# Kernel tuning notes

Measured on AMD Instinct MI355X. Metric: run time of the kernel, lower is better.

Reference implementation:

```python
import jax, jax.numpy as jnp
import numpy as np

B, S, D, H = 4, 2048, 1024, 16
DH = D // H
DFF = 4 * D
EPS = 1e-7


def _layernorm(x, scale, shift):
    # Note original quirk: (normalized + shift) * scale, biased variance, eps=1e-7
    m = jnp.mean(x, axis=-1, keepdims=True)
    v = jnp.mean((x - m) ** 2, axis=-1, keepdims=True)
    return ((x - m) / jnp.sqrt(v + EPS) + shift) * scale


def _gelu(x):
    c = jnp.sqrt(jnp.asarray(2.0 / jnp.pi, dtype=x.dtype))
    return 0.5 * x * (1.0 + jnp.tanh(c * (x + 0.044715 * x ** 3)))


def setup_inputs() -> dict:
    key = jax.random.key(0)
    ks = jax.random.split(key, 8)
    s = 0.02
    return {
        "x": jax.random.normal(ks[0], (B, S, D), jnp.float32),
        "Wq": jax.random.normal(ks[1], (D, D), jnp.float32) * s,
        "Wk": jax.random.normal(ks[2], (D, D), jnp.float32) * s,
        "Wv": jax.random.normal(ks[3], (D, D), jnp.float32) * s,
        "Wo": jax.random.normal(ks[4], (D, D), jnp.float32) * s,
        "bo": jnp.zeros((D,), jnp.float32),
        "W1": jax.random.normal(ks[5], (DFF, D), jnp.float32) * s,
        "b1": jnp.zeros((DFF,), jnp.float32),
        "W2": jax.random.normal(ks[6], (D, DFF), jnp.float32) * s,
        "b2": jnp.zeros((D,), jnp.float32),
        "ln1_scale": jnp.ones((D,), jnp.float32),
        "ln1_shift": jnp.zeros((D,), jnp.float32),
        "ln2_scale": jnp.ones((D,), jnp.float32),
        "ln2_shift": jnp.zeros((D,), jnp.float32),
    }


def reference(x, Wq, Wk, Wv, Wo, bo, W1, b1, W2, b2,
              ln1_scale, ln1_shift, ln2_scale, ln2_shift):
    b, s, d = x.shape
    h = _layernorm(x, ln1_scale, ln1_shift)
    # torch Linear: y = h @ W.T
    q = (h @ Wq.T).reshape(b, s, H, DH).transpose(0, 2, 1, 3)  # bhsd
    k = (h @ Wk.T).reshape(b, s, H, DH).transpose(0, 2, 1, 3)
    v = (h @ Wv.T).reshape(b, s, H, DH).transpose(0, 2, 1, 3)
    scores = jnp.einsum('bhqd,bhkd->bhqk', q, k) / jnp.sqrt(jnp.asarray(DH, x.dtype))
    causal = jnp.tril(jnp.ones((s, s), dtype=bool))
    scores = jnp.where(causal, scores, -jnp.inf)
    attn = jax.nn.softmax(scores, axis=-1)
    ctx = jnp.einsum('bhqk,bhkd->bhqd', attn, v)
    ctx = ctx.transpose(0, 2, 1, 3).reshape(b, s, d)
    attn_out = ctx @ Wo.T + bo
    x1 = x + attn_out  # residual (dropout is identity at eval / p effectively unused)
    h2 = _layernorm(x1, ln2_scale, ln2_shift)
    ff = _gelu(h2 @ W1.T + b1) @ W2.T + b2
    return x1 + ff
```

## Files before the change

kernel.cpp:

```cpp
#include <hip/hip_runtime.h>
#include <hip/hip_bf16.h>
#include <math.h>

typedef __bf16 bf16;
typedef __bf16 bf16x2_t __attribute__((ext_vector_type(2)));
typedef __bf16 bf16x4_t __attribute__((ext_vector_type(4)));
typedef __bf16 bf16x8_t __attribute__((ext_vector_type(8)));
typedef float  floatx4  __attribute__((ext_vector_type(4)));

#define DEVI static __device__ __forceinline__

constexpr int Bb = 4, Ss = 2048, Dd = 1024, Hh = 16, DHh = 64, DFFc = 4096;
constexpr int NTOK = Bb * Ss;
constexpr int NQKV = 3072;

DEVI void gld_lds16(const void* g, void* l) {
  __builtin_amdgcn_global_load_lds(
      (const __attribute__((address_space(1))) void*)g,
      (__attribute__((address_space(3))) void*)l, 16, 0, 0);
}

DEVI float gelu_f(float x) {
  const float c = 0.7978845608028654f;
  float t = tanhf(c * (x + 0.044715f * x * x * x));
  return 0.5f * x * (1.0f + t);
}

DEVI int xcd_lin(int lin, int nwg) {
  return (lin & 7) * (nwg >> 3) + (lin >> 3);
}

struct CastArgs {
  const float* src[6];
  bf16* dst[6];
  int n[6];
};
__global__ __launch_bounds__(256) void cast_w_kernel(CastArgs a) {
  const int which = blockIdx.y;
  const int idx = (blockIdx.x * 256 + threadIdx.x) * 4;
  if (idx >= a.n[which]) return;
  float4 v = *(const float4*)(a.src[which] + idx);
  bf16x4_t o = {(bf16)v.x, (bf16)v.y, (bf16)v.z, (bf16)v.w};
  *(bf16x4_t*)(a.dst[which] + idx) = o;
}

template <typename TIN>
__global__ __launch_bounds__(256) void ln_kernel(const TIN* __restrict__ x,
                                                 const float* __restrict__ sc,
                                                 const float* __restrict__ sh,
                                                 bf16* __restrict__ out) {
  __shared__ float rs[4], rs2[4];
  const int row = blockIdx.x, t = threadIdx.x;
  const TIN* xr = x + (size_t)row * Dd;
  float v[4];
  if constexpr (sizeof(TIN) == 2) {
    bf16x4_t tmp = *(const bf16x4_t*)((const bf16*)xr + t * 4);
#pragma unroll
    for (int i = 0; i < 4; i++) v[i] = (float)tmp[i];
  } else {
    float4 tmp = *(const float4*)((const float*)xr + t * 4);
    v[0] = tmp.x; v[1] = tmp.y; v[2] = tmp.z; v[3] = tmp.w;
  }
  float s = v[0] + v[1] + v[2] + v[3];
  float s2 = v[0] * v[0] + v[1] * v[1] + v[2] * v[2] + v[3] * v[3];
#pragma unroll
  for (int off = 1; off < 64; off <<= 1) {
    s += __shfl_xor(s, off);
    s2 += __shfl_xor(s2, off);
  }
  if ((t & 63) == 0) { rs[t >> 6] = s; rs2[t >> 6] = s2; }
  __syncthreads();
  float S1 = rs[0] + rs[1] + rs[2] + rs[3];
  float S2 = rs2[0] + rs2[1] + rs2[2] + rs2[3];
  float mean = S1 * (1.0f / Dd);
  float var = S2 * (1.0f / Dd) - mean * mean;
  float rinv = rsqrtf(var + 1e-7f);
#pragma unroll
  for (int i = 0; i < 4; i++) {
    int c = t * 4 + i;
    out[(size_t)row * Dd + c] = (bf16)(((v[i] - mean) * rinv + sh[c]) * sc[c]);
  }
}

template <int BN, int MODE>
__global__ __launch_bounds__(512, 2) void gemmk(const bf16* __restrict__ A,
                                                const bf16* __restrict__ Bw,
                                                const float* __restrict__ bias,
                                                const void* __restrict__ res,
                                                void* __restrict__ outp,
                                                int M, int N, int K) {
  constexpr int BUNITS = BN / 64;
  constexpr int AELEM = 16384;
  constexpr int BELEM = BUNITS * 4096;
  constexpr int WN = (BN == 256) ? 4 : 2;
  constexpr int WM = 8 / WN;
  constexpr int WR_H = 256 / WM;
  constexpr int M_rep = WR_H / 16;
  constexpr int NPH = M_rep / 2;
  __shared__ bf16 lds[2 * (AELEM + BELEM)];
  bf16* Ab = lds;
  bf16* Bl = lds + 2 * AELEM;

  const int tid = threadIdx.x;
  const int w = tid >> 6, lane = tid & 63;
  const int quad = lane >> 4, l16 = lane & 15;
  const int l7x8 = (lane & 7) << 3;
  const int wr = w / WN, wc = w % WN;

  const int gx = (int)gridDim.x;
  const int nwg = gx * (int)gridDim.y;
  const int lin = xcd_lin((int)blockIdx.y * gx + (int)blockIdx.x, nwg);
  const int m0 = (lin / gx) * 256;
  const int n0 = (lin % gx) * BN;

  const int s0 = w * 1024 + lane * 16;
  const int sr = s0 >> 7;
  const int sc = ((s0 ^ ((sr & 7) << 4)) & 127) >> 1;
  const int toff = w * 512 + lane * 8;

  const bf16* Agu[4];
  const bf16* Bgu[BUNITS];
#pragma unroll
  for (int u = 0; u < 4; ++u) Agu[u] = A + (size_t)(m0 + u * 64 + sr) * K + sc;
#pragma unroll
  for (int u = 0; u < BUNITS; ++u)
    Bgu[u] = Bw + (size_t)(n0 + u * 64 + sr) * K + sc;

  auto issA = [&](int t, int lo) {
    const int q = t & 1, ko = t * 64;
#pragma unroll
    for (int u = 0; u < 2; ++u)
      gld_lds16(Agu[lo + u] + ko, Ab + q * AELEM + (lo + u) * 4096 + toff);
  };
  auto issB = [&](int t, int lo, int cnt) {
    const int q = t & 1, ko = t * 64;
#pragma unroll 2
    for (int u = 0; u < cnt; ++u)
      gld_lds16(Bgu[lo + u] + ko, Bl + q * BELEM + (lo + u) * 4096 + toff);
  };

  auto rdA = [&](int q, int mi, int kk) {
    const int r = wr * WR_H + mi * 16 + l16;
    return *(const bf16x8_t*)(Ab + q * AELEM + (r >> 6) * 4096 + (r & 63) * 64 +
                              ((quad * 8 + kk * 32) ^ l7x8));
  };
  auto rdB = [&](int q, int j, int kk) {
    const int r = wc * 64 + j * 16 + l16;
    return *(const bf16x8_t*)(Bl + q * BELEM + (r >> 6) * 4096 + (r & 63) * 64 +
                              ((quad * 8 + kk * 32) ^ l7x8));
  };

  floatx4 acc[M_rep][4] = {};
  const int NT = K >> 6;

  issA(0, 0); issA(0, 2); issB(0, 0, BUNITS);
  issA(1, 0);
  if (BN == 256) {
    issB(1, 0, 2);
    asm volatile("s_waitcnt vmcnt(4)" ::: "memory");
  } else {
    asm volatile("s_waitcnt vmcnt(2)" ::: "memory");
  }
  __builtin_amdgcn_sched_barrier(0);
  __builtin_amdgcn_s_barrier();
  __builtin_amdgcn_sched_barrier(0);

  for (int t = 0; t < NT; ++t) {
    const int q = t & 1;
    bf16x8_t bfv[4][2];
#pragma unroll
    for (int p = 0; p < NPH; ++p) {
      bf16x8_t af[2][2];
#pragma unroll
      for (int im = 0; im < 2; ++im)
#pragma unroll
        for (int kk = 0; kk < 2; ++kk)
          af[im][kk] = rdA(q, p * 2 + im, kk);
      if (p == 0) {
#pragma unroll
        for (int j = 0; j < 4; ++j)
#pragma unroll
          for (int kk = 0; kk < 2; ++kk)
            bfv[j][kk] = rdB(q, j, kk);
        if (t + 1 < NT) {
          issA(t + 1, 2);
          if (BN == 256) issB(t + 1, 2, 2);
          else issB(t + 1, 0, 2);
        }
      }
      __builtin_amdgcn_s_barrier();
      __builtin_amdgcn_sched_barrier(0);
      __builtin_amdgcn_s_setprio(1);
#pragma unroll
      for (int im = 0; im < 2; ++im)
#pragma unroll
        for (int j = 0; j < 4; ++j)
#pragma unroll
          for (int kk = 0; kk < 2; ++kk)
            acc[p * 2 + im][j] = __builtin_amdgcn_mfma_f32_16x16x32_bf16(
                af[im][kk], bfv[j][kk], acc[p * 2 + im][j], 0, 0, 0);
      __builtin_amdgcn_s_setprio(0);
      if (p == NPH - 1) {
        if (t + 2 < NT) {
          issA(t + 2, 0);
          if (BN == 256) issB(t + 2, 0, 2);
          if (BN == 256) asm volatile("s_waitcnt vmcnt(4)" ::: "memory");
          else           asm volatile("s_waitcnt vmcnt(2)" ::: "memory");
        } else {
          asm volatile("s_waitcnt vmcnt(0)" ::: "memory");
        }
        __builtin_amdgcn_sched_barrier(0);
      }
      __builtin_amdgcn_s_barrier();
      __builtin_amdgcn_sched_barrier(0);
    }
  }

#pragma unroll
  for (int i = 0; i < M_rep; ++i) {
    const int rbase = m0 + wr * WR_H + i * 16 + quad * 4;
#pragma unroll
    for (int j2 = 0; j2 < 4; ++j2) {
      const int col = n0 + wc * 64 + j2 * 16 + l16;
      float bv = 0.f;
      if constexpr (MODE == 1 || MODE == 2 || MODE == 3) bv = bias[col];
#pragma unroll
      for (int r = 0; r < 4; ++r) {
        const int row = rbase + r;
        float vacc = acc[i][j2][r] + bv;
        if constexpr (MODE == 0) {
          ((bf16*)outp)[(size_t)row * N + col] = (bf16)vacc;
        } else if constexpr (MODE == 1) {
          float xres = ((const float*)res)[(size_t)row * N + col];
          ((bf16*)outp)[(size_t)row * N + col] = (bf16)(xres + vacc);
        } else if constexpr (MODE == 2) {
          ((bf16*)outp)[(size_t)row * N + col] = (bf16)gelu_f(vacc);
        } else {
          float xres = (float)((const bf16*)res)[(size_t)row * N + col];
          ((float*)outp)[(size_t)row * N + col] = xres + vacc;
        }
      }
    }
  }
}

__global__ __launch_bounds__(256) void attn_kernel(const bf16* __restrict__ QKV,
                                                   bf16* __restrict__ ctx) {
  __shared__ bf16 Ks[64 * 72];
  __shared__ bf16 Vt[64 * 72];
  __shared__ bf16 Ps[4][16 * 72];

  const int tid = threadIdx.x;
  const int wave = tid >> 6, lane = tid & 63;
  const int quad = lane >> 4, l16 = lane & 15;
  const int lin = xcd_lin((int)blockIdx.y * 16 + (int)blockIdx.x, 16 * Bb * Hh);
  const int qb = lin & 15;
  const int bh = lin >> 4;
  const int bsel = bh >> 4, hsel = bh & 15;
  const size_t base = ((size_t)bsel * Ss) * NQKV + (size_t)hsel * 64;
  const bf16* Qp = QKV + base;
  const bf16* Kp = QKV + base + 1024;
  const bf16* Vp = QKV + base + 2048;

  const int kr0 = tid >> 3, kc0 = (tid & 7) * 8;
  const int vp2 = tid & 31, vs = tid >> 5;

  for (int t = 0; t < 2; t++) {
    const int qt = (t == 0) ? qb : 31 - qb;
    const int q0 = qt * 64;

    const int qrow = q0 + wave * 16 + l16;
    bf16x8_t qf0 = *(const bf16x8_t*)(Qp + (size_t)qrow * NQKV + quad * 8);
    bf16x8_t qf1 = *(const bf16x8_t*)(Qp + (size_t)qrow * NQKV + 32 + quad * 8);
#pragma unroll
    for (int i = 0; i < 8; i++) {
      qf0[i] = (bf16)((float)qf0[i] * 0.125f);
      qf1[i] = (bf16)((float)qf1[i] * 0.125f);
    }

    floatx4 o[4] = {};
    float l_i[4] = {0.f, 0.f, 0.f, 0.f};

    {
      bf16x8_t k0 = *(const bf16x8_t*)(Kp + (size_t)kr0 * NQKV + kc0);
      bf16x8_t k1 = *(const bf16x8_t*)(Kp + (size_t)(kr0 + 32) * NQKV + kc0);
      const bf16* v0p = Vp + (size_t)(2 * vp2) * NQKV + vs * 8;
      bf16x8_t va = *(const bf16x8_t*)(v0p);
      bf16x8_t vb = *(const bf16x8_t*)(v0p + NQKV);
      *(bf16x8_t*)(Ks + kr0 * 72 + kc0) = k0;
      *(bf16x8_t*)(Ks + (kr0 + 32) * 72 + kc0) = k1;
#pragma unroll
      for (int i = 0; i < 8; i++) {
        bf16x2_t p2 = {va[i], vb[i]};
        *(bf16x2_t*)(Vt + (vs * 8 + i) * 72 + 2 * vp2) = p2;
      }
      __syncthreads();
    }

    const int ntiles = qt + 1;
    for (int it = 0; it < ntiles; ++it) {
      const int kc = it * 64;
      const bool more = (it + 1) < ntiles;

      bf16x8_t nk0, nk1, nva, nvb;
      if (more) {
        const int kn = kc + 64;
        nk0 = *(const bf16x8_t*)(Kp + (size_t)(kn + kr0) * NQKV + kc0);
        nk1 = *(const bf16x8_t*)(Kp + (size_t)(kn + kr0 + 32) * NQKV + kc0);
        const bf16* v0p = Vp + (size_t)(kn + 2 * vp2) * NQKV + vs * 8;
        nva = *(const bf16x8_t*)(v0p);
        nvb = *(const bf16x8_t*)(v0p + NQKV);
      }

      floatx4 sg[4];
      __builtin_amdgcn_s_setprio(1);
#pragma unroll
      for (int g = 0; g < 4; g++) {
        floatx4 s = {0.f, 0.f, 0.f, 0.f};
        bf16x8_t ka = *(const bf16x8_t*)(Ks + (g * 16 + l16) * 72 + quad * 8);
        bf16x8_t kb = *(const bf16x8_t*)(Ks + (g * 16 + l16) * 72 + 32 + quad * 8);
        s = __builtin_amdgcn_mfma_f32_16x16x32_bf16(qf0, ka, s, 0, 0, 0);
        s = __builtin_amdgcn_mfma_f32_16x16x32_bf16(qf1, kb, s, 0, 0, 0);
        sg[g] = s;
      }
      __builtin_amdgcn_s_setprio(0);

      bf16* pw = &Ps[wave][0];
      const bool diag = (kc == q0);
      if (diag) {
#pragma unroll
        for (int r = 0; r < 4; r++) {
          const int rq = q0 + wave * 16 + quad * 4 + r;
          float p[4];
          float rsum = 0.f;
#pragma unroll
          for (int g = 0; g < 4; g++) {
            float v = (kc + g * 16 + l16 > rq) ? -1e30f : sg[g][r];
            p[g] = __expf(v);
            rsum += p[g];
          }
          rsum += __shfl_xor(rsum, 1);
          rsum += __shfl_xor(rsum, 2);
          rsum += __shfl_xor(rsum, 4);
          rsum += __shfl_xor(rsum, 8);
          l_i[r] += rsum;
#pragma unroll
          for (int g = 0; g < 4; g++)
            pw[(quad * 4 + r) * 72 + g * 16 + l16] = (bf16)p[g];
        }
      } else {
#pragma unroll
        for (int r = 0; r < 4; r++) {
          float p[4];
          float rsum = 0.f;
#pragma unroll
          for (int g = 0; g < 4; g++) {
            p[g] = __expf(sg[g][r]);
            rsum += p[g];
          }
          rsum += __shfl_xor(rsum, 1);
          rsum += __shfl_xor(rsum, 2);
          rsum += __shfl_xor(rsum, 4);
          rsum += __shfl_xor(rsum, 8);
          l_i[r] += rsum;
#pragma unroll
          for (int g = 0; g < 4; g++)
            pw[(quad * 4 + r) * 72 + g * 16 + l16] = (bf16)p[g];
        }
      }

      bf16x8_t pf0 = *(const bf16x8_t*)(pw + l16 * 72 + quad * 8);
      bf16x8_t pf1 = *(const bf16x8_t*)(pw + l16 * 72 + 32 + quad * 8);
      __builtin_amdgcn_s_setprio(1);
#pragma unroll
      for (int nt = 0; nt < 4; nt++) {
        bf16x8_t vf0 = *(const bf16x8_t*)(Vt + (nt * 16 + l16) * 72 + quad * 8);
        bf16x8_t vf1 = *(const bf16x8_t*)(Vt + (nt * 16 + l16) * 72 + 32 + quad * 8);
        o[nt] = __builtin_amdgcn_mfma_f32_16x16x32_bf16(pf0, vf0, o[nt], 0, 0, 0);
        o[nt] = __builtin_amdgcn_mfma_f32_16x16x32_bf16(pf1, vf1, o[nt], 0, 0, 0);
      }
      __builtin_amdgcn_s_setprio(0);

      __syncthreads();
      if (more) {
        *(bf16x8_t*)(Ks + kr0 * 72 + kc0) = nk0;
        *(bf16x8_t*)(Ks + (kr0 + 32) * 72 + kc0) = nk1;
#pragma unroll
        for (int i = 0; i < 8; i++) {
          bf16x2_t p2 = {nva[i], nvb[i]};
          *(bf16x2_t*)(Vt + (vs * 8 + i) * 72 + 2 * vp2) = p2;
        }
        __syncthreads();
      }
    }

#pragma unroll
    for (int nt = 0; nt < 4; nt++)
#pragma unroll
      for (int r = 0; r < 4; r++) {
        const int rq = q0 + wave * 16 + quad * 4 + r;
        size_t a = ((size_t)bsel * Ss + rq) * Dd + (size_t)hsel * DHh + nt * 16 + l16;
        ctx[a] = (bf16)(o[nt][r] / l_i[r]);
      }
  }
}

extern "C" void kernel_launch(void* const* d_in, const int* in_sizes, int n_in,
                              void* d_out, int out_size, void* d_ws, size_t ws_size,
                              hipStream_t stream) {
  (void)in_sizes; (void)n_in; (void)out_size; (void)ws_size;
  const float* x = (const float*)d_in[0];
  const float* Wq = (const float*)d_in[1];
  const float* Wk = (const float*)d_in[2];
  const float* Wv = (const float*)d_in[3];
  const float* Wo = (const float*)d_in[4];
  const float* bo = (const float*)d_in[5];
  const float* W1 = (const float*)d_in[6];
  const float* b1 = (const float*)d_in[7];
  const float* W2 = (const float*)d_in[8];
  const float* b2 = (const float*)d_in[9];
  const float* ln1s = (const float*)d_in[10];
  const float* ln1b = (const float*)d_in[11];
  const float* ln2s = (const float*)d_in[12];
  const float* ln2b = (const float*)d_in[13];

  char* wsb = (char*)d_ws;
  const size_t MB = 1024 * 1024;
  bf16* Wqb = (bf16*)(wsb);
  bf16* Wkb = (bf16*)(wsb + 2 * MB);
  bf16* Wvb = (bf16*)(wsb + 4 * MB);
  bf16* Wob = (bf16*)(wsb + 6 * MB);
  bf16* W1b = (bf16*)(wsb + 8 * MB);
  bf16* W2b = (bf16*)(wsb + 16 * MB);
  bf16* h   = (bf16*)(wsb + 24 * MB);
  bf16* qkv = (bf16*)(wsb + 40 * MB);
  bf16* ctx = (bf16*)(wsb + 88 * MB);
  bf16* x1  = (bf16*)(wsb + 104 * MB);
  bf16* h2  = ctx;
  bf16* ff1 = h;

  dim3 blk(256, 1, 1);
  dim3 blk8(512, 1, 1);

  CastArgs ca;
  ca.src[0] = Wq; ca.src[1] = Wk; ca.src[2] = Wv; ca.src[3] = Wo;
  ca.src[4] = W1; ca.src[5] = W2;
  ca.dst[0] = Wqb; ca.dst[1] = Wkb; ca.dst[2] = Wvb; ca.dst[3] = Wob;
  ca.dst[4] = W1b; ca.dst[5] = W2b;
  ca.n[0] = ca.n[1] = ca.n[2] = ca.n[3] = Dd * Dd;
  ca.n[4] = ca.n[5] = Dd * DFFc;
  cast_w_kernel<<<dim3((Dd * DFFc) / (256 * 4), 6, 1), blk, 0, stream>>>(ca);

  ln_kernel<float><<<dim3(NTOK, 1, 1), blk, 0, stream>>>(x, ln1s, ln1b, h);
  gemmk<256, 0><<<dim3(12, NTOK / 256, 1), blk8, 0, stream>>>(h, Wqb, nullptr, nullptr,
                                                              qkv, NTOK, NQKV, Dd);
  attn_kernel<<<dim3(16, Bb * Hh, 1), blk, 0, stream>>>(qkv, ctx);
  gemmk<128, 1><<<dim3(8, NTOK / 256, 1), blk8, 0, stream>>>(ctx, Wob, bo, x, x1,
                                                             NTOK, Dd, Dd);
  ln_kernel<bf16><<<dim3(NTOK, 1, 1), blk, 0, stream>>>(x1, ln2s, ln2b, h2);
  gemmk<256, 2><<<dim3(16, NTOK / 256, 1), blk8, 0, stream>>>(h2, W1b, b1, nullptr, ff1,
                                                              NTOK, DFFc, Dd);
  gemmk<128, 3><<<dim3(8, NTOK / 256, 1), blk8, 0, stream>>>(ff1, W2b, b2, x1,
                                                             (float*)d_out, NTOK, Dd, DFFc);
}
```

Baseline: 506.9 us.

## Process two adjacent query tiles per attention block to reuse K/V tiles

Each attention block now handles two consecutive 64-row query tiles at once, sharing every staged K/V tile in LDS between both, and balances work by pairing tile group g with 15-g. This halves K/V global loads and LDS staging per query row and halves the grid to 512 blocks. In exchange it raises register pressure (two sets of Q fragments, accumulators and scores), doubles the P scratch in LDS, and lowers the number of blocks available to hide latency.

```diff
diff --git a/kernel.cpp b/kernel.cpp
--- a/kernel.cpp
+++ b/kernel.cpp
@@ -248,14 +248,14 @@
                                                    bf16* __restrict__ ctx) {
   __shared__ bf16 Ks[64 * 72];
   __shared__ bf16 Vt[64 * 72];
-  __shared__ bf16 Ps[4][16 * 72];
+  __shared__ bf16 Ps[4][2][16 * 72];
 
   const int tid = threadIdx.x;
   const int wave = tid >> 6, lane = tid & 63;
   const int quad = lane >> 4, l16 = lane & 15;
-  const int lin = xcd_lin((int)blockIdx.y * 16 + (int)blockIdx.x, 16 * Bb * Hh);
-  const int qb = lin & 15;
-  const int bh = lin >> 4;
+  const int lin = xcd_lin((int)blockIdx.y * 8 + (int)blockIdx.x, 8 * Bb * Hh);
+  const int gsel = lin & 7;
+  const int bh = lin >> 3;
   const int bsel = bh >> 4, hsel = bh & 15;
   const size_t base = ((size_t)bsel * Ss) * NQKV + (size_t)hsel * 64;
   const bf16* Qp = QKV + base;
@@ -265,21 +265,27 @@
   const int kr0 = tid >> 3, kc0 = (tid & 7) * 8;
   const int vp2 = tid & 31, vs = tid >> 5;
 
-  for (int t = 0; t < 2; t++) {
-    const int qt = (t == 0) ? qb : 31 - qb;
-    const int q0 = qt * 64;
-
-    const int qrow = q0 + wave * 16 + l16;
-    bf16x8_t qf0 = *(const bf16x8_t*)(Qp + (size_t)qrow * NQKV + quad * 8);
-    bf16x8_t qf1 = *(const bf16x8_t*)(Qp + (size_t)qrow * NQKV + 32 + quad * 8);
+  for (int pass = 0; pass < 2; ++pass) {
+    const int g2 = (pass == 0) ? gsel : 15 - gsel;
+    const int tA = 2 * g2, tB = tA + 1;
+    const int q0A = tA * 64, q0B = q0A + 64;
+
+    const int qrA = q0A + wave * 16 + l16;
+    const int qrB = q0B + wave * 16 + l16;
+    bf16x8_t qA0 = *(const bf16x8_t*)(Qp + (size_t)qrA * NQKV + quad * 8);
+    bf16x8_t qA1 = *(const bf16x8_t*)(Qp + (size_t)qrA * NQKV + 32 + quad * 8);
+    bf16x8_t qB0 = *(const bf16x8_t*)(Qp + (size_t)qrB * NQKV + quad * 8);
+    bf16x8_t qB1 = *(const bf16x8_t*)(Qp + (size_t)qrB * NQKV + 32 + quad * 8);
 #pragma unroll
     for (int i = 0; i < 8; i++) {
-      qf0[i] = (bf16)((float)qf0[i] * 0.125f);
-      qf1[i] = (bf16)((float)qf1[i] * 0.125f);
+      qA0[i] = (bf16)((float)qA0[i] * 0.125f);
+      qA1[i] = (bf16)((float)qA1[i] * 0.125f);
+      qB0[i] = (bf16)((float)qB0[i] * 0.125f);
+      qB1[i] = (bf16)((float)qB1[i] * 0.125f);
     }
 
-    floatx4 o[4] = {};
-    float l_i[4] = {0.f, 0.f, 0.f, 0.f};
+    floatx4 oA[4] = {}, oB[4] = {};
+    float lA[4] = {0.f, 0.f, 0.f, 0.f}, lB[4] = {0.f, 0.f, 0.f, 0.f};
 
     {
       bf16x8_t k0 = *(const bf16x8_t*)(Kp + (size_t)kr0 * NQKV + kc0);
@@ -297,40 +303,12 @@
       __syncthreads();
     }
 
-    const int ntiles = qt + 1;
-    for (int it = 0; it < ntiles; ++it) {
-      const int kc = it * 64;
-      const bool more = (it + 1) < ntiles;
-
-      bf16x8_t nk0, nk1, nva, nvb;
-      if (more) {
-        const int kn = kc + 64;
-        nk0 = *(const bf16x8_t*)(Kp + (size_t)(kn + kr0) * NQKV + kc0);
-        nk1 = *(const bf16x8_t*)(Kp + (size_t)(kn + kr0 + 32) * NQKV + kc0);
-        const bf16* v0p = Vp + (size_t)(kn + 2 * vp2) * NQKV + vs * 8;
-        nva = *(const bf16x8_t*)(v0p);
-        nvb = *(const bf16x8_t*)(v0p + NQKV);
-      }
-
-      floatx4 sg[4];
-      __builtin_amdgcn_s_setprio(1);
-#pragma unroll
-      for (int g = 0; g < 4; g++) {
-        floatx4 s = {0.f, 0.f, 0.f, 0.f};
-        bf16x8_t ka = *(const bf16x8_t*)(Ks + (g * 16 + l16) * 72 + quad * 8);
-        bf16x8_t kb = *(const bf16x8_t*)(Ks + (g * 16 + l16) * 72 + 32 + quad * 8);
-        s = __builtin_amdgcn_mfma_f32_16x16x32_bf16(qf0, ka, s, 0, 0, 0);
-        s = __builtin_amdgcn_mfma_f32_16x16x32_bf16(qf1, kb, s, 0, 0, 0);
-        sg[g] = s;
-      }
-      __builtin_amdgcn_s_setprio(0);
-
-      bf16* pw = &Ps[wave][0];
-      const bool diag = (kc == q0);
+    auto do_sm = [&](floatx4* sg, float* l_i, bf16* pw, int q0c, bool diag,
+                     int kc) {
       if (diag) {
 #pragma unroll
         for (int r = 0; r < 4; r++) {
-          const int rq = q0 + wave * 16 + quad * 4 + r;
+          const int rq = q0c + wave * 16 + quad * 4 + r;
           float p[4];
           float rsum = 0.f;
 #pragma unroll
@@ -368,16 +346,61 @@
             pw[(quad * 4 + r) * 72 + g * 16 + l16] = (bf16)p[g];
         }
       }
-
-      bf16x8_t pf0 = *(const bf16x8_t*)(pw + l16 * 72 + quad * 8);
-      bf16x8_t pf1 = *(const bf16x8_t*)(pw + l16 * 72 + 32 + quad * 8);
+    };
+
+    const int ntiles = tB + 1;
+    for (int it = 0; it < ntiles; ++it) {
+      const int kc = it * 64;
+      const bool more = (it + 1) < ntiles;
+      const bool aAct = (it <= tA);
+
+      bf16x8_t nk0, nk1, nva, nvb;
+      if (more) {
+        const int kn = kc + 64;
+        nk0 = *(const bf16x8_t*)(Kp + (size_t)(kn + kr0) * NQKV + kc0);
+        nk1 = *(const bf16x8_t*)(Kp + (size_t)(kn + kr0 + 32) * NQKV + kc0);
+        const bf16* v0p = Vp + (size_t)(kn + 2 * vp2) * NQKV + vs * 8;
+        nva = *(const bf16x8_t*)(v0p);
+        nvb = *(const bf16x8_t*)(v0p + NQKV);
+      }
+
+      floatx4 sA[4], sB[4];
+      __builtin_amdgcn_s_setprio(1);
+#pragma unroll
+      for (int g = 0; g < 4; g++) {
+        bf16x8_t ka = *(const bf16x8_t*)(Ks + (g * 16 + l16) * 72 + quad * 8);
+        bf16x8_t kb = *(const bf16x8_t*)(Ks + (g * 16 + l16) * 72 + 32 + quad * 8);
+        floatx4 z = {0.f, 0.f, 0.f, 0.f};
+        if (aAct) {
+          floatx4 s = __builtin_amdgcn_mfma_f32_16x16x32_bf16(qA0, ka, z, 0, 0, 0);
+          sA[g] = __builtin_amdgcn_mfma_f32_16x16x32_bf16(qA1, kb, s, 0, 0, 0);
+        }
+        floatx4 s2 = __builtin_amdgcn_mfma_f32_16x16x32_bf16(qB0, ka, z, 0, 0, 0);
+        sB[g] = __builtin_amdgcn_mfma_f32_16x16x32_bf16(qB1, kb, s2, 0, 0, 0);
+      }
+      __builtin_amdgcn_s_setprio(0);
+
+      if (aAct) do_sm(sA, lA, &Ps[wave][0][0], q0A, it == tA, kc);
+      do_sm(sB, lB, &Ps[wave][1][0], q0B, it == tB, kc);
+
+      bf16x8_t pA0, pA1;
+      if (aAct) {
+        pA0 = *(const bf16x8_t*)(&Ps[wave][0][0] + l16 * 72 + quad * 8);
+        pA1 = *(const bf16x8_t*)(&Ps[wave][0][0] + l16 * 72 + 32 + quad * 8);
+      }
+      bf16x8_t pB0 = *(const bf16x8_t*)(&Ps[wave][1][0] + l16 * 72 + quad * 8);
+      bf16x8_t pB1 = *(const bf16x8_t*)(&Ps[wave][1][0] + l16 * 72 + 32 + quad * 8);
       __builtin_amdgcn_s_setprio(1);
 #pragma unroll
       for (int nt = 0; nt < 4; nt++) {
         bf16x8_t vf0 = *(const bf16x8_t*)(Vt + (nt * 16 + l16) * 72 + quad * 8);
         bf16x8_t vf1 = *(const bf16x8_t*)(Vt + (nt * 16 + l16) * 72 + 32 + quad * 8);
-        o[nt] = __builtin_amdgcn_mfma_f32_16x16x32_bf16(pf0, vf0, o[nt], 0, 0, 0);
-        o[nt] = __builtin_amdgcn_mfma_f32_16x16x32_bf16(pf1, vf1, o[nt], 0, 0, 0);
+        if (aAct) {
+          oA[nt] = __builtin_amdgcn_mfma_f32_16x16x32_bf16(pA0, vf0, oA[nt], 0, 0, 0);
+          oA[nt] = __builtin_amdgcn_mfma_f32_16x16x32_bf16(pA1, vf1, oA[nt], 0, 0, 0);
+        }
+        oB[nt] = __builtin_amdgcn_mfma_f32_16x16x32_bf16(pB0, vf0, oB[nt], 0, 0, 0);
+        oB[nt] = __builtin_amdgcn_mfma_f32_16x16x32_bf16(pB1, vf1, oB[nt], 0, 0, 0);
       }
       __builtin_amdgcn_s_setprio(0);
 
@@ -398,9 +421,12 @@
     for (int nt = 0; nt < 4; nt++)
 #pragma unroll
       for (int r = 0; r < 4; r++) {
-        const int rq = q0 + wave * 16 + quad * 4 + r;
-        size_t a = ((size_t)bsel * Ss + rq) * Dd + (size_t)hsel * DHh + nt * 16 + l16;
-        ctx[a] = (bf16)(o[nt][r] / l_i[r]);
+        const int rqA = q0A + wave * 16 + quad * 4 + r;
+        const int rqB = q0B + wave * 16 + quad * 4 + r;
+        size_t aa = ((size_t)bsel * Ss + rqA) * Dd + (size_t)hsel * DHh + nt * 16 + l16;
+        size_t ab = ((size_t)bsel * Ss + rqB) * Dd + (size_t)hsel * DHh + nt * 16 + l16;
+        ctx[aa] = (bf16)(oA[nt][r] / lA[r]);
+        ctx[ab] = (bf16)(oB[nt][r] / lB[r]);
       }
   }
 }
@@ -454,7 +480,7 @@
   ln_kernel<float><<<dim3(NTOK, 1, 1), blk, 0, stream>>>(x, ln1s, ln1b, h);
   gemmk<256, 0><<<dim3(12, NTOK / 256, 1), blk8, 0, stream>>>(h, Wqb, nullptr, nullptr,
                                                               qkv, NTOK, NQKV, Dd);
-  attn_kernel<<<dim3(16, Bb * Hh, 1), blk, 0, stream>>>(qkv, ctx);
+  attn_kernel<<<dim3(8, Bb * Hh, 1), blk, 0, stream>>>(qkv, ctx);
   gemmk<128, 1><<<dim3(8, NTOK / 256, 1), blk8, 0, stream>>>(ctx, Wob, bo, x, x1,
                                                              NTOK, Dd, Dd);
   ln_kernel<bf16><<<dim3(NTOK, 1, 1), blk, 0, stream>>>(x1, ln2s, ln2b, h2);
```

After: 493.0 us. 2.7% less time.
